# Kernel tuning notes

Hardware: AMD Instinct MI355X
Metric: run time of the kernel (lower is better)

## Reference

```python
import jax, jax.numpy as jnp
import numpy as np

N_NODES = 50000
N_EDGES = 800000
N_GRAPHS = 512
NEG_SLOPE = 0.2  # PyG GATConv default LeakyReLU slope


def _gat_layer(x, src, dst, W, a_src, a_dst, b, n_nodes):
    """PyG-style GATConv (concat=True, self-loops already in src/dst)."""
    H, C = a_src.shape
    h = (x @ W).reshape(n_nodes, H, C)            # [N, H, C]
    e_s = (h * a_src).sum(-1)                     # [N, H]
    e_d = (h * a_dst).sum(-1)                     # [N, H]
    e = jax.nn.leaky_relu(e_s[src] + e_d[dst], NEG_SLOPE)  # [E, H]
    # segment softmax over destination nodes
    m = jax.ops.segment_max(e, dst, num_segments=n_nodes)
    w = jnp.exp(e - m[dst])
    s = jax.ops.segment_sum(w, dst, num_segments=n_nodes)
    alpha = w / (s[dst] + 1e-16)                  # [E, H]
    out = jax.ops.segment_sum(h[src] * alpha[:, :, None], dst, num_segments=n_nodes)
    return out.reshape(n_nodes, H * C) + b


def setup_inputs() -> dict:
    key = jax.random.key(0)
    ks = jax.random.split(key, 16)
    x = jax.random.normal(ks[0], (N_NODES, 2), dtype=jnp.float32)
    edge_index = jax.random.randint(ks[1], (2, N_EDGES), 0, N_NODES, dtype=jnp.int64 if jax.config.jax_enable_x64 else jnp.int32)
    batch = jnp.sort(jax.random.randint(ks[2], (N_NODES,), 0, N_GRAPHS))
    g = lambda k, shape: (jax.random.normal(k, shape, dtype=jnp.float32) * 0.1)
    return {
        "x": x, "edge_index": edge_index, "batch": batch,
        "W1": g(ks[3], (2, 64)),   "a1s": g(ks[4], (8, 8)),  "a1d": g(ks[5], (8, 8)),  "b1": jnp.zeros((64,), jnp.float32),
        "W2": g(ks[6], (64, 128)), "a2s": g(ks[7], (8, 16)), "a2d": g(ks[8], (8, 16)), "b2": jnp.zeros((128,), jnp.float32),
        "W3": g(ks[9], (128, 128)),"a3s": g(ks[10], (8, 16)),"a3d": g(ks[11], (8, 16)),"b3": jnp.zeros((128,), jnp.float32),
        "fc1W": g(ks[12], (128, 32)), "fc1b": jnp.zeros((32,), jnp.float32),
        "fc2W": g(ks[13], (32, 10)),  "fc2b": jnp.zeros((10,), jnp.float32),
    }


def reference(x, edge_index, batch, W1, a1s, a1d, b1, W2, a2s, a2d, b2, W3, a3s, a3d, b3, fc1W, fc1b, fc2W, fc2b):
    n = x.shape[0]
    loop = jnp.arange(n, dtype=edge_index.dtype)
    src = jnp.concatenate([edge_index[0], loop])  # add self-loops (PyG default)
    dst = jnp.concatenate([edge_index[1], loop])
    h = jax.nn.elu(_gat_layer(x, src, dst, W1, a1s, a1d, b1, n))
    h = jax.nn.elu(_gat_layer(h, src, dst, W2, a2s, a2d, b2, n))
    h = _gat_layer(h, src, dst, W3, a3s, a3d, b3, n)
    # global mean pool over graphs
    sums = jax.ops.segment_sum(h, batch, num_segments=N_GRAPHS)
    cnt = jax.ops.segment_sum(jnp.ones((n,), h.dtype), batch, num_segments=N_GRAPHS)
    pooled = sums / jnp.maximum(cnt, 1.0)[:, None]   # [G, 128]
    z = jax.nn.relu(pooled @ fc1W + fc1b)
    return jax.nn.log_softmax(z @ fc2W + fc2b, axis=1)
```

## Files before the change

### kernel.cpp

```cpp
#include <hip/hip_runtime.h>
#include <cstddef>
#include <cstdint>

typedef __attribute__((ext_vector_type(8))) short bf16x8;
typedef __attribute__((ext_vector_type(4))) float floatx4;
typedef __attribute__((ext_vector_type(2))) float v2f;


__device__ __forceinline__ unsigned bf16pair(float a, float b) {
    unsigned ua = __float_as_uint(a), ub = __float_as_uint(b);
    ua += 0x7fffu + ((ua >> 16) & 1u);
    ub += 0x7fffu + ((ub >> 16) & 1u);
    return (ua >> 16) | (ub & 0xffff0000u);
}
__device__ __forceinline__ unsigned short bf16one(float a) {
    unsigned ua = __float_as_uint(a);
    ua += 0x7fffu + ((ua >> 16) & 1u);
    return (unsigned short)(ua >> 16);
}

#define BSTRIDE 8192


__global__ __launch_bounds__(256) void prep_k(
    const int* __restrict__ edge, unsigned* __restrict__ barr,
    int* __restrict__ bcnt, int E, int EA, int B1,
    const float* __restrict__ W2, unsigned short* __restrict__ Wt2,
    const float* __restrict__ W3, unsigned short* __restrict__ Wt3,
    const float* __restrict__ x, const float* __restrict__ W1,
    const float* __restrict__ a1s, const float* __restrict__ a1d,
    unsigned char* __restrict__ h8a, float* __restrict__ es,
    float* __restrict__ ed, int N) {
    int tid = threadIdx.x;
    if ((int)blockIdx.x < B1) {
        __shared__ int h[256];
        __shared__ int lbase[256];
        h[tid] = 0;
        __syncthreads();
        int start = blockIdx.x * 4096;
        unsigned ent[16];
        int lp[16];
#pragma unroll
        for (int k = 0; k < 16; ++k) {
            int i = start + k * 256 + tid;
            if (i < EA) {
                int s, d;
                if (i < E) { s = edge[i]; d = edge[E + i]; }
                else { s = i - E; d = s; }
                int b = d >> 8;
                ent[k] = (unsigned)s | ((unsigned)(d & 255) << 16) | ((unsigned)b << 24);
                lp[k] = atomicAdd(&h[b], 1);
            } else {
                ent[k] = 0xffffffffu;
                lp[k] = 0;
            }
        }
        __syncthreads();
        lbase[tid] = h[tid] ? atomicAdd(&bcnt[tid], h[tid]) : 0;
        __syncthreads();
#pragma unroll
        for (int k = 0; k < 16; ++k) {
            if (ent[k] != 0xffffffffu) {
                int b = ent[k] >> 24;
                int pos = lbase[b] + lp[k];
                if (pos < BSTRIDE)
                    barr[(size_t)b * BSTRIDE + pos] = ent[k] & 0x00ffffffu;
            }
        }
        return;
    }
    if ((int)blockIdx.x < B1 + 96) {
        int rel = blockIdx.x - B1;
        const float* W = (rel < 32) ? W2 : W3;
        unsigned short* Wt = (rel < 32) ? Wt2 : Wt3;
        int total = (rel < 32) ? 8192 : 16384;
        int o = ((rel < 32) ? rel : rel - 32) * 256 + tid;
        if (o < total) {
            int j = o & 7, lane = (o >> 3) & 63, ct = (o >> 9) & 7, ks = o >> 12;
            int k = ks * 32 + (lane >> 4) * 8 + j;
            int n = ct * 16 + (lane & 15);
            Wt[o] = bf16one(W[k * 128 + n]);
        }
        return;
    }
    int wave = tid >> 6, lane = tid & 63;
    int nbase = (blockIdx.x - B1 - 96) * 32;
    float w0 = W1[lane], w1 = W1[64 + lane];
    float as = a1s[lane], ad = a1d[lane];
    int head = lane >> 3;
#pragma unroll
    for (int it = 0; it < 8; ++it) {
        int n = nbase + it * 4 + wave;
        int nc = (n < N) ? n : N - 1;
        float2 xv = ((const float2*)x)[nc];
        float h = xv.x * w0 + xv.y * w1;
        float ps = h * as, pd = h * ad;
#pragma unroll
        for (int off = 1; off < 8; off <<= 1) {
            ps += __shfl_xor(ps, off);
            pd += __shfl_xor(pd, off);
        }
        if (n < N) {
            unsigned d = __builtin_amdgcn_cvt_pk_fp8_f32(h, h, 0, false);
            h8a[(size_t)n * 64 + lane] = (unsigned char)d;
            if ((lane & 7) == 0) { es[n * 8 + head] = ps; ed[n * 8 + head] = pd; }
        }
    }
}


__global__ __launch_bounds__(256) void bucket2_k(const unsigned* __restrict__ barr,
                                                 const int* __restrict__ bcnt,
                                                 int* __restrict__ offsets,
                                                 int* __restrict__ esrc,
                                                 int N, int EA, int nbuck) {
    __shared__ int sd[256];
    __shared__ int bb[256];
    __shared__ int cur[256];
    int b = blockIdx.x, tid = threadIdx.x;
    int v = (tid < nbuck) ? bcnt[tid] : 0;
    sd[tid] = v;
    __syncthreads();
    for (int off = 1; off < 256; off <<= 1) {
        int t = (tid >= off) ? sd[tid - off] : 0;
        __syncthreads();
        sd[tid] += t;
        __syncthreads();
    }
    bb[tid] = sd[tid] - v;
    __syncthreads();
    int bbase = bb[b];
    if (b == 0 && tid == 0) offsets[N] = EA;
    if (b == 0 && tid < 8) esrc[EA + tid] = 0;

    int cnt = bcnt[b];
    const unsigned* arr = barr + (size_t)b * BSTRIDE;
    sd[tid] = 0;
    __syncthreads();
    for (int i = tid; i < cnt; i += 256)
        atomicAdd(&sd[(arr[i] >> 16) & 0xff], 1);
    __syncthreads();
    v = sd[tid];
    for (int off = 1; off < 256; off <<= 1) {
        int t = (tid >= off) ? sd[tid - off] : 0;
        __syncthreads();
        sd[tid] += t;
        __syncthreads();
    }
    int base = bbase + sd[tid] - v;
    int n = b * 256 + tid;
    if (n < N) offsets[n] = base;
    cur[tid] = base;
    __syncthreads();
    for (int i = tid; i < cnt; i += 256) {
        unsigned e = arr[i];
        int pos = atomicAdd(&cur[(e >> 16) & 0xff], 1);
        esrc[pos] = (int)(e & 0xffffu);
    }
}


template <int IN>
__global__ __launch_bounds__(256) void gemm_mfma_k(
    const unsigned short* __restrict__ a16, const unsigned short* __restrict__ Wt,
    const float* __restrict__ a_s, const float* __restrict__ a_d,
    unsigned char* __restrict__ h8, float* __restrict__ es, float* __restrict__ ed,
    int n_nodes) {
    constexpr int KSTEPS = IN / 32;
    __shared__ float Cl[64 * 132];
    int wave = threadIdx.x >> 6, lane = threadIdx.x & 63;
    int q = lane >> 4, m = lane & 15;
    int rbase = blockIdx.x * 64;

    floatx4 acc[8];
#pragma unroll
    for (int ct = 0; ct < 8; ++ct) acc[ct] = (floatx4){0.f, 0.f, 0.f, 0.f};

    int ra = rbase + wave * 16 + m;
    if (ra >= n_nodes) ra = n_nodes - 1;
    const unsigned short* arow = a16 + (size_t)ra * IN + q * 8;

#pragma unroll
    for (int ks = 0; ks < KSTEPS; ++ks) {
        bf16x8 af = *(const bf16x8*)(arow + ks * 32);
        const unsigned short* wp = Wt + ((size_t)(ks * 8) * 64 + lane) * 8;
#pragma unroll
        for (int ct = 0; ct < 8; ++ct) {
            bf16x8 bf = *(const bf16x8*)(wp + (size_t)ct * 64 * 8);
            acc[ct] = __builtin_amdgcn_mfma_f32_16x16x32_bf16(af, bf, acc[ct], 0, 0, 0);
        }
    }

#pragma unroll
    for (int ct = 0; ct < 8; ++ct)
#pragma unroll
        for (int i = 0; i < 4; ++i)
            Cl[(wave * 16 + q * 4 + i) * 132 + ct * 16 + m] = acc[ct][i];
    __syncthreads();

    int rl = threadIdx.x >> 2, part = threadIdx.x & 3;
    int r = rbase + rl;
    if (r < n_nodes) {
        const float* cp = &Cl[rl * 132 + part * 32];
        float e0s = 0.f, e0d = 0.f, e1s = 0.f, e1d = 0.f;
#pragma unroll
        for (int c = 0; c < 16; ++c) {
            float v = cp[c];
            int ai = part * 32 + c;
            e0s += v * a_s[ai];
            e0d += v * a_d[ai];
        }
#pragma unroll
        for (int c = 16; c < 32; ++c) {
            float v = cp[c];
            int ai = part * 32 + c;
            e1s += v * a_s[ai];
            e1d += v * a_d[ai];
        }
        unsigned pk8[8];
#pragma unroll
        for (int u = 0; u < 8; ++u) {
            unsigned d = __builtin_amdgcn_cvt_pk_fp8_f32(cp[4 * u], cp[4 * u + 1], 0, false);
            d = __builtin_amdgcn_cvt_pk_fp8_f32(cp[4 * u + 2], cp[4 * u + 3], d, true);
            pk8[u] = d;
        }
        uint4* hp = (uint4*)(h8 + (size_t)r * 128) + part * 2;
        hp[0] = make_uint4(pk8[0], pk8[1], pk8[2], pk8[3]);
        hp[1] = make_uint4(pk8[4], pk8[5], pk8[6], pk8[7]);
        es[r * 8 + 2 * part] = e0s;
        es[r * 8 + 2 * part + 1] = e1s;
        ed[r * 8 + 2 * part] = e0d;
        ed[r * 8 + 2 * part + 1] = e1d;
    }
}


template <int NCOL, bool ELU>
__global__ __launch_bounds__(256) void gat_k(
    const unsigned char* __restrict__ hsrc, const float* __restrict__ es,
    const float* __restrict__ ed, const int* __restrict__ offsets,
    const int* __restrict__ esrc, const float* __restrict__ bias,
    void* __restrict__ outp, int n_nodes) {
    constexpr int UPL = NCOL / 16;
    int wave = threadIdx.x >> 6, lane = threadIdx.x & 63;
    int half = lane >> 5;
    int hl = lane & 31;
    int slot = hl >> 3;
    int l = lane & 7;
    int n = blockIdx.x * 8 + wave * 2 + half;
    bool valid = (n < n_nodes);
    int nc = valid ? n : 0;
    float edn = ed[nc * 8 + l];
    int start = valid ? offsets[nc] : 0;
    int end = valid ? offsets[nc + 1] : 0;

    v2f acc2[UPL];
#pragma unroll
    for (int k = 0; k < UPL; ++k) acc2[k] = (v2f){0.f, 0.f};
    float s = 0.f;

    for (int j = start; j < end; j += 4) {
        int jj = j + slot;
        bool act = (jj < end);
        int src = esrc[jj];
        float e0 = es[(size_t)src * 8 + l] + edn;
        float e = fmaxf(e0, 0.2f * e0);
        float p = act ? __expf(e) : 0.f;
        s += p;
        v2f p2 = (v2f){p, p};
        if constexpr (NCOL == 128) {
            uint4 u = *(const uint4*)(hsrc + (size_t)src * 128 + 16 * l);
            acc2[0] += p2 * (v2f)__builtin_amdgcn_cvt_pk_f32_fp8(u.x, false);
            acc2[1] += p2 * (v2f)__builtin_amdgcn_cvt_pk_f32_fp8(u.x, true);
            acc2[2] += p2 * (v2f)__builtin_amdgcn_cvt_pk_f32_fp8(u.y, false);
            acc2[3] += p2 * (v2f)__builtin_amdgcn_cvt_pk_f32_fp8(u.y, true);
            acc2[4] += p2 * (v2f)__builtin_amdgcn_cvt_pk_f32_fp8(u.z, false);
            acc2[5] += p2 * (v2f)__builtin_amdgcn_cvt_pk_f32_fp8(u.z, true);
            acc2[6] += p2 * (v2f)__builtin_amdgcn_cvt_pk_f32_fp8(u.w, false);
            acc2[7] += p2 * (v2f)__builtin_amdgcn_cvt_pk_f32_fp8(u.w, true);
        } else {
            uint2 u = *(const uint2*)(hsrc + (size_t)src * 64 + 8 * l);
            acc2[0] += p2 * (v2f)__builtin_amdgcn_cvt_pk_f32_fp8(u.x, false);
            acc2[1] += p2 * (v2f)__builtin_amdgcn_cvt_pk_f32_fp8(u.x, true);
            acc2[2] += p2 * (v2f)__builtin_amdgcn_cvt_pk_f32_fp8(u.y, false);
            acc2[3] += p2 * (v2f)__builtin_amdgcn_cvt_pk_f32_fp8(u.y, true);
        }
    }

    s += __shfl_xor(s, 8);
    s += __shfl_xor(s, 16);
    float v[2 * UPL];
#pragma unroll
    for (int k = 0; k < UPL; ++k) { v[2 * k] = acc2[k].x; v[2 * k + 1] = acc2[k].y; }
#pragma unroll
    for (int k = 0; k < 2 * UPL; ++k) {
        v[k] += __shfl_xor(v[k], 8);
        v[k] += __shfl_xor(v[k], 16);
    }

    if (slot == 0 && valid) {
        float r = 1.f / (s + 1e-16f);
#pragma unroll
        for (int k = 0; k < 2 * UPL; ++k) {
            float b = bias[(2 * UPL) * l + k];
            float t = v[k] * r + b;
            if constexpr (ELU) t = (t > 0.f) ? t : expm1f(t);
            v[k] = t;
        }
        if constexpr (NCOL == 128) {
            uint4* op = (uint4*)outp + (size_t)n * 16 + 2 * l;
            op[0] = make_uint4(bf16pair(v[0], v[1]), bf16pair(v[2], v[3]),
                               bf16pair(v[4], v[5]), bf16pair(v[6], v[7]));
            op[1] = make_uint4(bf16pair(v[8], v[9]), bf16pair(v[10], v[11]),
                               bf16pair(v[12], v[13]), bf16pair(v[14], v[15]));
        } else {
            ((uint4*)outp)[(size_t)n * 8 + l] =
                make_uint4(bf16pair(v[0], v[1]), bf16pair(v[2], v[3]),
                           bf16pair(v[4], v[5]), bf16pair(v[6], v[7]));
        }
    }
}


__global__ __launch_bounds__(64) void pool_k(const unsigned* __restrict__ hu,
                                             const int* __restrict__ batch,
                                             float* __restrict__ sums,
                                             float* __restrict__ cnt, int n_nodes) {
    int c = threadIdx.x;
    int base = blockIdx.x * 32;
    float a0 = 0.f, a1 = 0.f, cacc = 0.f;
    int gprev = -1;
    for (int k = 0; k < 32; k++) {
        int n = base + k;
        if (n >= n_nodes) break;
        int g = batch[n];
        if (g != gprev) {
            if (gprev >= 0) {
                atomicAdd(&sums[gprev * 128 + 2 * c], a0);
                atomicAdd(&sums[gprev * 128 + 2 * c + 1], a1);
                if (c == 0) atomicAdd(&cnt[gprev], cacc);
            }
            a0 = 0.f; a1 = 0.f; cacc = 0.f; gprev = g;
        }
        unsigned u = hu[(size_t)n * 64 + c];
        a0 += __uint_as_float(u << 16);
        a1 += __uint_as_float(u & 0xffff0000u);
        cacc += 1.f;
    }
    if (gprev >= 0) {
        atomicAdd(&sums[gprev * 128 + 2 * c], a0);
        atomicAdd(&sums[gprev * 128 + 2 * c + 1], a1);
        if (c == 0) atomicAdd(&cnt[gprev], cacc);
    }
}


__global__ __launch_bounds__(64) void fc_k(const float* __restrict__ sums,
                                           const float* __restrict__ cnt,
                                           const float* __restrict__ fc1W,
                                           const float* __restrict__ fc1b,
                                           const float* __restrict__ fc2W,
                                           const float* __restrict__ fc2b,
                                           float* __restrict__ out) {
    int g = blockIdx.x, lane = threadIdx.x;
    __shared__ float p[128];
    __shared__ float z[32];
    __shared__ float logits[10];
    float inv = 1.f / fmaxf(cnt[g], 1.f);
    p[lane] = sums[g * 128 + lane] * inv;
    p[lane + 64] = sums[g * 128 + 64 + lane] * inv;
    __syncthreads();
    if (lane < 32) {
        float a = fc1b[lane];
        for (int k = 0; k < 128; k++) a += p[k] * fc1W[k * 32 + lane];
        z[lane] = fmaxf(a, 0.f);
    }
    __syncthreads();
    if (lane < 10) {
        float a = fc2b[lane];
        for (int k = 0; k < 32; k++) a += z[k] * fc2W[k * 10 + lane];
        logits[lane] = a;
    }
    __syncthreads();
    if (lane < 10) {
        float mx = logits[0];
#pragma unroll
        for (int i = 1; i < 10; i++) mx = fmaxf(mx, logits[i]);
        float se = 0.f;
#pragma unroll
        for (int i = 0; i < 10; i++) se += __expf(logits[i] - mx);
        out[g * 10 + lane] = logits[lane] - mx - logf(se);
    }
}


extern "C" void kernel_launch(void* const* d_in, const int* in_sizes, int n_in,
                              void* d_out, int out_size, void* d_ws, size_t ws_size,
                              hipStream_t stream) {
    const float* x = (const float*)d_in[0];
    const int* edge = (const int*)d_in[1];
    const int* batch = (const int*)d_in[2];
    const float* W1 = (const float*)d_in[3];
    const float* a1s = (const float*)d_in[4];
    const float* a1d = (const float*)d_in[5];
    const float* b1 = (const float*)d_in[6];
    const float* W2 = (const float*)d_in[7];
    const float* a2s = (const float*)d_in[8];
    const float* a2d = (const float*)d_in[9];
    const float* b2 = (const float*)d_in[10];
    const float* W3 = (const float*)d_in[11];
    const float* a3s = (const float*)d_in[12];
    const float* a3d = (const float*)d_in[13];
    const float* b3 = (const float*)d_in[14];
    const float* fc1W = (const float*)d_in[15];
    const float* fc1b = (const float*)d_in[16];
    const float* fc2W = (const float*)d_in[17];
    const float* fc2b = (const float*)d_in[18];
    float* out = (float*)d_out;

    const int N = in_sizes[0] / 2;
    const int E = in_sizes[1] / 2;
    const int EA = E + N;
    const int NG = out_size / 10;
    const int NBUCK = (N + 255) >> 8;
    const int B1 = (EA + 4095) / 4096;
    const int G1 = (N + 31) / 32;

    char* p = (char*)d_ws;
    unsigned* h3b16 = (unsigned*)p; p += (size_t)N * 64 * 4;
    unsigned char* h8 = (unsigned char*)p; p += (size_t)N * 128;
    unsigned char* h8a = (unsigned char*)p; p += (size_t)N * 64;
    unsigned short* a16a = (unsigned short*)p; p += (size_t)N * 64 * 2;
    unsigned short* a16b = (unsigned short*)p; p += (size_t)N * 128 * 2;
    unsigned short* Wt2 = (unsigned short*)p; p += (size_t)64 * 128 * 2;
    unsigned short* Wt3 = (unsigned short*)p; p += (size_t)128 * 128 * 2;
    float* es = (float*)p;  p += (size_t)N * 8 * 4;
    float* ed = (float*)p;  p += (size_t)N * 8 * 4;
    float* sums = (float*)p; p += (size_t)NG * 128 * 4;
    float* cnt = (float*)p;  p += (size_t)NG * 4;
    int* bcnt = (int*)p;     p += 256 * 4;
    int* offsets = (int*)p;  p += (size_t)(N + 1) * 4;
    int* esrc = (int*)p;     p += (size_t)(EA + 8) * 4;
    unsigned* barr = (unsigned*)p; p += (size_t)NBUCK * BSTRIDE * 4;

    hipMemsetAsync(sums, 0, ((size_t)NG * 128 + NG + 256) * 4, stream);

    prep_k<<<B1 + 96 + G1, 256, 0, stream>>>(
        edge, barr, bcnt, E, EA, B1, W2, Wt2, W3, Wt3,
        x, W1, a1s, a1d, h8a, es, ed, N);
    bucket2_k<<<NBUCK, 256, 0, stream>>>(barr, bcnt, offsets, esrc, N, EA, NBUCK);

    int mblocks = (N + 63) / 64;
    int ablocks = (N + 7) / 8;
    gat_k<64, true><<<ablocks, 256, 0, stream>>>(h8a, es, ed, offsets, esrc, b1, a16a, N);
    gemm_mfma_k<64><<<mblocks, 256, 0, stream>>>(a16a, Wt2, a2s, a2d, h8, es, ed, N);
    gat_k<128, true><<<ablocks, 256, 0, stream>>>(h8, es, ed, offsets, esrc, b2, a16b, N);
    gemm_mfma_k<128><<<mblocks, 256, 0, stream>>>(a16b, Wt3, a3s, a3d, h8, es, ed, N);
    gat_k<128, false><<<ablocks, 256, 0, stream>>>(h8, es, ed, offsets, esrc, b3, h3b16, N);

    pool_k<<<(N + 31) / 32, 64, 0, stream>>>(h3b16, batch, sums, cnt, N);
    fc_k<<<NG, 64, 0, stream>>>(sums, cnt, fc1W, fc1b, fc2W, fc2b, out);
}
```

Baseline: 278.3 us.

## Fuse all stages into one cooperative persistent kernel with grid syncs

```diff
diff --git a/kernel.cpp b/kernel.cpp
--- a/kernel.cpp
+++ b/kernel.cpp
@@ -1,10 +1,16 @@
 #include <hip/hip_runtime.h>
+#include <hip/hip_cooperative_groups.h>
 #include <cstddef>
 #include <cstdint>
+
+namespace cg = cooperative_groups;
 
 typedef __attribute__((ext_vector_type(8))) short bf16x8;
 typedef __attribute__((ext_vector_type(4))) float floatx4;
 typedef __attribute__((ext_vector_type(2))) float v2f;
+
+#define BSTRIDE 8192
+#define SMEM_BYTES (64 * 132 * 4)
 
 
 __device__ __forceinline__ unsigned bf16pair(float a, float b) {
@@ -19,34 +25,46 @@
     return (unsigned short)(ua >> 16);
 }
 
-#define BSTRIDE 8192
-
-
-__global__ __launch_bounds__(256) void prep_k(
-    const int* __restrict__ edge, unsigned* __restrict__ barr,
-    int* __restrict__ bcnt, int E, int EA, int B1,
-    const float* __restrict__ W2, unsigned short* __restrict__ Wt2,
-    const float* __restrict__ W3, unsigned short* __restrict__ Wt3,
-    const float* __restrict__ x, const float* __restrict__ W1,
-    const float* __restrict__ a1s, const float* __restrict__ a1d,
-    unsigned char* __restrict__ h8a, float* __restrict__ es,
-    float* __restrict__ ed, int N) {
+
+struct MA {
+    const int* edge;
+    unsigned* barr;
+    int* bcnt;
+    int E, EA, B1, PREP, NBUCK, N, NG, ablocks, mblocks, pblocks;
+    const float *W1, *W2, *W3;
+    unsigned short *Wt2, *Wt3;
+    const float* x;
+    const float *a1s, *a1d, *a2s, *a2d, *a3s, *a3d;
+    const float *b1, *b2, *b3;
+    unsigned char *h8a, *h8;
+    unsigned short *a16a, *a16b;
+    unsigned* h3b16;
+    float *es, *ed;
+    int *offsets, *esrc;
+    const int* batch;
+    float *sums, *cnt;
+    const float *fc1W, *fc1b, *fc2W, *fc2b;
+    float* out;
+};
+
+
+__device__ void prep_body(int vb, const MA& a, char* smem) {
     int tid = threadIdx.x;
-    if ((int)blockIdx.x < B1) {
-        __shared__ int h[256];
-        __shared__ int lbase[256];
+    if (vb < a.B1) {
+        int* h = (int*)smem;
+        int* lbase = h + 256;
         h[tid] = 0;
         __syncthreads();
-        int start = blockIdx.x * 4096;
+        int start = vb * 4096;
         unsigned ent[16];
         int lp[16];
 #pragma unroll
         for (int k = 0; k < 16; ++k) {
             int i = start + k * 256 + tid;
-            if (i < EA) {
+            if (i < a.EA) {
                 int s, d;
-                if (i < E) { s = edge[i]; d = edge[E + i]; }
-                else { s = i - E; d = s; }
+                if (i < a.E) { s = a.edge[i]; d = a.edge[a.E + i]; }
+                else { s = i - a.E; d = s; }
                 int b = d >> 8;
                 ent[k] = (unsigned)s | ((unsigned)(d & 255) << 16) | ((unsigned)b << 24);
                 lp[k] = atomicAdd(&h[b], 1);
@@ -56,7 +74,7 @@
             }
         }
         __syncthreads();
-        lbase[tid] = h[tid] ? atomicAdd(&bcnt[tid], h[tid]) : 0;
+        lbase[tid] = h[tid] ? atomicAdd(&a.bcnt[tid], h[tid]) : 0;
         __syncthreads();
 #pragma unroll
         for (int k = 0; k < 16; ++k) {
@@ -64,15 +82,16 @@
                 int b = ent[k] >> 24;
                 int pos = lbase[b] + lp[k];
                 if (pos < BSTRIDE)
-                    barr[(size_t)b * BSTRIDE + pos] = ent[k] & 0x00ffffffu;
+                    a.barr[(size_t)b * BSTRIDE + pos] = ent[k] & 0x00ffffffu;
             }
         }
+        __syncthreads();
         return;
     }
-    if ((int)blockIdx.x < B1 + 96) {
-        int rel = blockIdx.x - B1;
-        const float* W = (rel < 32) ? W2 : W3;
-        unsigned short* Wt = (rel < 32) ? Wt2 : Wt3;
+    if (vb < a.B1 + 96) {
+        int rel = vb - a.B1;
+        const float* W = (rel < 32) ? a.W2 : a.W3;
+        unsigned short* Wt = (rel < 32) ? a.Wt2 : a.Wt3;
         int total = (rel < 32) ? 8192 : 16384;
         int o = ((rel < 32) ? rel : rel - 32) * 256 + tid;
         if (o < total) {
@@ -84,15 +103,15 @@
         return;
     }
     int wave = tid >> 6, lane = tid & 63;
-    int nbase = (blockIdx.x - B1 - 96) * 32;
-    float w0 = W1[lane], w1 = W1[64 + lane];
-    float as = a1s[lane], ad = a1d[lane];
+    int nbase = (vb - a.B1 - 96) * 32;
+    float w0 = a.W1[lane], w1 = a.W1[64 + lane];
+    float as = a.a1s[lane], ad = a.a1d[lane];
     int head = lane >> 3;
 #pragma unroll
     for (int it = 0; it < 8; ++it) {
         int n = nbase + it * 4 + wave;
-        int nc = (n < N) ? n : N - 1;
-        float2 xv = ((const float2*)x)[nc];
+        int nc = (n < a.N) ? n : a.N - 1;
+        float2 xv = ((const float2*)a.x)[nc];
         float h = xv.x * w0 + xv.y * w1;
         float ps = h * as, pd = h * ad;
 #pragma unroll
@@ -100,25 +119,20 @@
             ps += __shfl_xor(ps, off);
             pd += __shfl_xor(pd, off);
         }
-        if (n < N) {
+        if (n < a.N) {
             unsigned d = __builtin_amdgcn_cvt_pk_fp8_f32(h, h, 0, false);
-            h8a[(size_t)n * 64 + lane] = (unsigned char)d;
-            if ((lane & 7) == 0) { es[n * 8 + head] = ps; ed[n * 8 + head] = pd; }
-        }
-    }
-}
-
-
-__global__ __launch_bounds__(256) void bucket2_k(const unsigned* __restrict__ barr,
-                                                 const int* __restrict__ bcnt,
-                                                 int* __restrict__ offsets,
-                                                 int* __restrict__ esrc,
-                                                 int N, int EA, int nbuck) {
-    __shared__ int sd[256];
-    __shared__ int bb[256];
-    __shared__ int cur[256];
-    int b = blockIdx.x, tid = threadIdx.x;
-    int v = (tid < nbuck) ? bcnt[tid] : 0;
+            a.h8a[(size_t)n * 64 + lane] = (unsigned char)d;
+            if ((lane & 7) == 0) { a.es[n * 8 + head] = ps; a.ed[n * 8 + head] = pd; }
+        }
+    }
+}
+
+__device__ void bucket2_body(int b, const MA& a, char* smem) {
+    int* sd = (int*)smem;
+    int* bb = sd + 256;
+    int* cur = bb + 256;
+    int tid = threadIdx.x;
+    int v = (tid < a.NBUCK) ? a.bcnt[tid] : 0;
     sd[tid] = v;
     __syncthreads();
     for (int off = 1; off < 256; off <<= 1) {
@@ -130,11 +144,11 @@
     bb[tid] = sd[tid] - v;
     __syncthreads();
     int bbase = bb[b];
-    if (b == 0 && tid == 0) offsets[N] = EA;
-    if (b == 0 && tid < 8) esrc[EA + tid] = 0;
-
-    int cnt = bcnt[b];
-    const unsigned* arr = barr + (size_t)b * BSTRIDE;
+    if (b == 0 && tid == 0) a.offsets[a.N] = a.EA;
+    if (b == 0 && tid < 8) a.esrc[a.EA + tid] = 0;
+
+    int cnt = a.bcnt[b];
+    const unsigned* arr = a.barr + (size_t)b * BSTRIDE;
     sd[tid] = 0;
     __syncthreads();
     for (int i = tid; i < cnt; i += 256)
@@ -149,105 +163,30 @@
     }
     int base = bbase + sd[tid] - v;
     int n = b * 256 + tid;
-    if (n < N) offsets[n] = base;
+    if (n < a.N) a.offsets[n] = base;
     cur[tid] = base;
     __syncthreads();
     for (int i = tid; i < cnt; i += 256) {
         unsigned e = arr[i];
         int pos = atomicAdd(&cur[(e >> 16) & 0xff], 1);
-        esrc[pos] = (int)(e & 0xffffu);
-    }
-}
-
-
-template <int IN>
-__global__ __launch_bounds__(256) void gemm_mfma_k(
-    const unsigned short* __restrict__ a16, const unsigned short* __restrict__ Wt,
-    const float* __restrict__ a_s, const float* __restrict__ a_d,
-    unsigned char* __restrict__ h8, float* __restrict__ es, float* __restrict__ ed,
-    int n_nodes) {
-    constexpr int KSTEPS = IN / 32;
-    __shared__ float Cl[64 * 132];
-    int wave = threadIdx.x >> 6, lane = threadIdx.x & 63;
-    int q = lane >> 4, m = lane & 15;
-    int rbase = blockIdx.x * 64;
-
-    floatx4 acc[8];
-#pragma unroll
-    for (int ct = 0; ct < 8; ++ct) acc[ct] = (floatx4){0.f, 0.f, 0.f, 0.f};
-
-    int ra = rbase + wave * 16 + m;
-    if (ra >= n_nodes) ra = n_nodes - 1;
-    const unsigned short* arow = a16 + (size_t)ra * IN + q * 8;
-
-#pragma unroll
-    for (int ks = 0; ks < KSTEPS; ++ks) {
-        bf16x8 af = *(const bf16x8*)(arow + ks * 32);
-        const unsigned short* wp = Wt + ((size_t)(ks * 8) * 64 + lane) * 8;
-#pragma unroll
-        for (int ct = 0; ct < 8; ++ct) {
-            bf16x8 bf = *(const bf16x8*)(wp + (size_t)ct * 64 * 8);
-            acc[ct] = __builtin_amdgcn_mfma_f32_16x16x32_bf16(af, bf, acc[ct], 0, 0, 0);
-        }
-    }
-
-#pragma unroll
-    for (int ct = 0; ct < 8; ++ct)
-#pragma unroll
-        for (int i = 0; i < 4; ++i)
-            Cl[(wave * 16 + q * 4 + i) * 132 + ct * 16 + m] = acc[ct][i];
-    __syncthreads();
-
-    int rl = threadIdx.x >> 2, part = threadIdx.x & 3;
-    int r = rbase + rl;
-    if (r < n_nodes) {
-        const float* cp = &Cl[rl * 132 + part * 32];
-        float e0s = 0.f, e0d = 0.f, e1s = 0.f, e1d = 0.f;
-#pragma unroll
-        for (int c = 0; c < 16; ++c) {
-            float v = cp[c];
-            int ai = part * 32 + c;
-            e0s += v * a_s[ai];
-            e0d += v * a_d[ai];
-        }
-#pragma unroll
-        for (int c = 16; c < 32; ++c) {
-            float v = cp[c];
-            int ai = part * 32 + c;
-            e1s += v * a_s[ai];
-            e1d += v * a_d[ai];
-        }
-        unsigned pk8[8];
-#pragma unroll
-        for (int u = 0; u < 8; ++u) {
-            unsigned d = __builtin_amdgcn_cvt_pk_fp8_f32(cp[4 * u], cp[4 * u + 1], 0, false);
-            d = __builtin_amdgcn_cvt_pk_fp8_f32(cp[4 * u + 2], cp[4 * u + 3], d, true);
-            pk8[u] = d;
-        }
-        uint4* hp = (uint4*)(h8 + (size_t)r * 128) + part * 2;
-        hp[0] = make_uint4(pk8[0], pk8[1], pk8[2], pk8[3]);
-        hp[1] = make_uint4(pk8[4], pk8[5], pk8[6], pk8[7]);
-        es[r * 8 + 2 * part] = e0s;
-        es[r * 8 + 2 * part + 1] = e1s;
-        ed[r * 8 + 2 * part] = e0d;
-        ed[r * 8 + 2 * part + 1] = e1d;
-    }
-}
-
+        a.esrc[pos] = (int)(e & 0xffffu);
+    }
+    __syncthreads();
+}
 
 template <int NCOL, bool ELU>
-__global__ __launch_bounds__(256) void gat_k(
-    const unsigned char* __restrict__ hsrc, const float* __restrict__ es,
-    const float* __restrict__ ed, const int* __restrict__ offsets,
-    const int* __restrict__ esrc, const float* __restrict__ bias,
-    void* __restrict__ outp, int n_nodes) {
+__device__ void gat_body(int vb, const unsigned char* __restrict__ hsrc,
+                         const float* __restrict__ es, const float* __restrict__ ed,
+                         const int* __restrict__ offsets, const int* __restrict__ esrc,
+                         const float* __restrict__ bias, void* __restrict__ outp,
+                         int n_nodes) {
     constexpr int UPL = NCOL / 16;
     int wave = threadIdx.x >> 6, lane = threadIdx.x & 63;
     int half = lane >> 5;
     int hl = lane & 31;
     int slot = hl >> 3;
     int l = lane & 7;
-    int n = blockIdx.x * 8 + wave * 2 + half;
+    int n = vb * 8 + wave * 2 + half;
     bool valid = (n < n_nodes);
     int nc = valid ? n : 0;
     float edn = ed[nc * 8 + l];
@@ -321,143 +260,280 @@
     }
 }
 
-
-__global__ __launch_bounds__(64) void pool_k(const unsigned* __restrict__ hu,
-                                             const int* __restrict__ batch,
-                                             float* __restrict__ sums,
-                                             float* __restrict__ cnt, int n_nodes) {
+template <int IN>
+__device__ void mfma_body(int vb, const unsigned short* __restrict__ a16,
+                          const unsigned short* __restrict__ Wt,
+                          const float* __restrict__ a_s, const float* __restrict__ a_d,
+                          unsigned char* __restrict__ h8, float* __restrict__ es,
+                          float* __restrict__ ed, int n_nodes, char* smem) {
+    constexpr int KSTEPS = IN / 32;
+    float* Cl = (float*)smem;
+    int wave = threadIdx.x >> 6, lane = threadIdx.x & 63;
+    int q = lane >> 4, m = lane & 15;
+    int rbase = vb * 64;
+
+    floatx4 acc[8];
+#pragma unroll
+    for (int ct = 0; ct < 8; ++ct) acc[ct] = (floatx4){0.f, 0.f, 0.f, 0.f};
+
+    int ra = rbase + wave * 16 + m;
+    if (ra >= n_nodes) ra = n_nodes - 1;
+    const unsigned short* arow = a16 + (size_t)ra * IN + q * 8;
+
+#pragma unroll
+    for (int ks = 0; ks < KSTEPS; ++ks) {
+        bf16x8 af = *(const bf16x8*)(arow + ks * 32);
+        const unsigned short* wp = Wt + ((size_t)(ks * 8) * 64 + lane) * 8;
+#pragma unroll
+        for (int ct = 0; ct < 8; ++ct) {
+            bf16x8 bf = *(const bf16x8*)(wp + (size_t)ct * 64 * 8);
+            acc[ct] = __builtin_amdgcn_mfma_f32_16x16x32_bf16(af, bf, acc[ct], 0, 0, 0);
+        }
+    }
+
+#pragma unroll
+    for (int ct = 0; ct < 8; ++ct)
+#pragma unroll
+        for (int i = 0; i < 4; ++i)
+            Cl[(wave * 16 + q * 4 + i) * 132 + ct * 16 + m] = acc[ct][i];
+    __syncthreads();
+
+    int rl = threadIdx.x >> 2, part = threadIdx.x & 3;
+    int r = rbase + rl;
+    if (r < n_nodes) {
+        const float* cp = &Cl[rl * 132 + part * 32];
+        float e0s = 0.f, e0d = 0.f, e1s = 0.f, e1d = 0.f;
+#pragma unroll
+        for (int c = 0; c < 16; ++c) {
+            float v = cp[c];
+            int ai = part * 32 + c;
+            e0s += v * a_s[ai];
+            e0d += v * a_d[ai];
+        }
+#pragma unroll
+        for (int c = 16; c < 32; ++c) {
+            float v = cp[c];
+            int ai = part * 32 + c;
+            e1s += v * a_s[ai];
+            e1d += v * a_d[ai];
+        }
+        unsigned pk8[8];
+#pragma unroll
+        for (int u = 0; u < 8; ++u) {
+            unsigned d = __builtin_amdgcn_cvt_pk_fp8_f32(cp[4 * u], cp[4 * u + 1], 0, false);
+            d = __builtin_amdgcn_cvt_pk_fp8_f32(cp[4 * u + 2], cp[4 * u + 3], d, true);
+            pk8[u] = d;
+        }
+        uint4* hp = (uint4*)(h8 + (size_t)r * 128) + part * 2;
+        hp[0] = make_uint4(pk8[0], pk8[1], pk8[2], pk8[3]);
+        hp[1] = make_uint4(pk8[4], pk8[5], pk8[6], pk8[7]);
+        es[r * 8 + 2 * part] = e0s;
+        es[r * 8 + 2 * part + 1] = e1s;
+        ed[r * 8 + 2 * part] = e0d;
+        ed[r * 8 + 2 * part + 1] = e1d;
+    }
+    __syncthreads();
+}
+
+__device__ void pool_body(int vb, const MA& a) {
     int c = threadIdx.x;
-    int base = blockIdx.x * 32;
+    if (c >= 64) return;
+    int base = vb * 32;
     float a0 = 0.f, a1 = 0.f, cacc = 0.f;
     int gprev = -1;
     for (int k = 0; k < 32; k++) {
         int n = base + k;
-        if (n >= n_nodes) break;
-        int g = batch[n];
+        if (n >= a.N) break;
+        int g = a.batch[n];
         if (g != gprev) {
             if (gprev >= 0) {
-                atomicAdd(&sums[gprev * 128 + 2 * c], a0);
-                atomicAdd(&sums[gprev * 128 + 2 * c + 1], a1);
-                if (c == 0) atomicAdd(&cnt[gprev], cacc);
+                atomicAdd(&a.sums[gprev * 128 + 2 * c], a0);
+                atomicAdd(&a.sums[gprev * 128 + 2 * c + 1], a1);
+                if (c == 0) atomicAdd(&a.cnt[gprev], cacc);
             }
             a0 = 0.f; a1 = 0.f; cacc = 0.f; gprev = g;
         }
-        unsigned u = hu[(size_t)n * 64 + c];
+        unsigned u = a.h3b16[(size_t)n * 64 + c];
         a0 += __uint_as_float(u << 16);
         a1 += __uint_as_float(u & 0xffff0000u);
         cacc += 1.f;
     }
     if (gprev >= 0) {
-        atomicAdd(&sums[gprev * 128 + 2 * c], a0);
-        atomicAdd(&sums[gprev * 128 + 2 * c + 1], a1);
-        if (c == 0) atomicAdd(&cnt[gprev], cacc);
-    }
-}
-
-
-__global__ __launch_bounds__(64) void fc_k(const float* __restrict__ sums,
-                                           const float* __restrict__ cnt,
-                                           const float* __restrict__ fc1W,
-                                           const float* __restrict__ fc1b,
-                                           const float* __restrict__ fc2W,
-                                           const float* __restrict__ fc2b,
-                                           float* __restrict__ out) {
-    int g = blockIdx.x, lane = threadIdx.x;
-    __shared__ float p[128];
-    __shared__ float z[32];
-    __shared__ float logits[10];
-    float inv = 1.f / fmaxf(cnt[g], 1.f);
-    p[lane] = sums[g * 128 + lane] * inv;
-    p[lane + 64] = sums[g * 128 + 64 + lane] * inv;
-    __syncthreads();
-    if (lane < 32) {
-        float a = fc1b[lane];
-        for (int k = 0; k < 128; k++) a += p[k] * fc1W[k * 32 + lane];
-        z[lane] = fmaxf(a, 0.f);
-    }
-    __syncthreads();
-    if (lane < 10) {
-        float a = fc2b[lane];
-        for (int k = 0; k < 32; k++) a += z[k] * fc2W[k * 10 + lane];
-        logits[lane] = a;
-    }
-    __syncthreads();
-    if (lane < 10) {
+        atomicAdd(&a.sums[gprev * 128 + 2 * c], a0);
+        atomicAdd(&a.sums[gprev * 128 + 2 * c + 1], a1);
+        if (c == 0) atomicAdd(&a.cnt[gprev], cacc);
+    }
+}
+
+__device__ void fc_body(int g, const MA& a, char* smem) {
+    float* p = (float*)smem;
+    float* z = p + 128;
+    float* logits = z + 32;
+    int tid = threadIdx.x;
+    if (tid < 64) {
+        float inv = 1.f / fmaxf(a.cnt[g], 1.f);
+        p[tid] = a.sums[g * 128 + tid] * inv;
+        p[tid + 64] = a.sums[g * 128 + 64 + tid] * inv;
+    }
+    __syncthreads();
+    if (tid < 32) {
+        float acc = a.fc1b[tid];
+        for (int k = 0; k < 128; k++) acc += p[k] * a.fc1W[k * 32 + tid];
+        z[tid] = fmaxf(acc, 0.f);
+    }
+    __syncthreads();
+    if (tid < 10) {
+        float acc = a.fc2b[tid];
+        for (int k = 0; k < 32; k++) acc += z[k] * a.fc2W[k * 10 + tid];
+        logits[tid] = acc;
+    }
+    __syncthreads();
+    if (tid < 10) {
         float mx = logits[0];
 #pragma unroll
         for (int i = 1; i < 10; i++) mx = fmaxf(mx, logits[i]);
         float se = 0.f;
 #pragma unroll
         for (int i = 0; i < 10; i++) se += __expf(logits[i] - mx);
-        out[g * 10 + lane] = logits[lane] - mx - logf(se);
-    }
+        a.out[g * 10 + tid] = logits[tid] - mx - logf(se);
+    }
+    __syncthreads();
+}
+
+
+__global__ __launch_bounds__(256) void mega_k(MA a) {
+    __shared__ __align__(16) char smem[SMEM_BYTES];
+    cg::grid_group grid = cg::this_grid();
+
+    for (int vb = blockIdx.x; vb < a.PREP; vb += gridDim.x) prep_body(vb, a, smem);
+    grid.sync();
+    for (int vb = blockIdx.x; vb < a.NBUCK; vb += gridDim.x) bucket2_body(vb, a, smem);
+    grid.sync();
+    for (int vb = blockIdx.x; vb < a.ablocks; vb += gridDim.x)
+        gat_body<64, true>(vb, a.h8a, a.es, a.ed, a.offsets, a.esrc, a.b1, a.a16a, a.N);
+    grid.sync();
+    for (int vb = blockIdx.x; vb < a.mblocks; vb += gridDim.x)
+        mfma_body<64>(vb, a.a16a, a.Wt2, a.a2s, a.a2d, a.h8, a.es, a.ed, a.N, smem);
+    grid.sync();
+    for (int vb = blockIdx.x; vb < a.ablocks; vb += gridDim.x)
+        gat_body<128, true>(vb, a.h8, a.es, a.ed, a.offsets, a.esrc, a.b2, a.a16b, a.N);
+    grid.sync();
+    for (int vb = blockIdx.x; vb < a.mblocks; vb += gridDim.x)
+        mfma_body<128>(vb, a.a16b, a.Wt3, a.a3s, a.a3d, a.h8, a.es, a.ed, a.N, smem);
+    grid.sync();
+    for (int vb = blockIdx.x; vb < a.ablocks; vb += gridDim.x)
+        gat_body<128, false>(vb, a.h8, a.es, a.ed, a.offsets, a.esrc, a.b3, a.h3b16, a.N);
+    grid.sync();
+    for (int vb = blockIdx.x; vb < a.pblocks; vb += gridDim.x) pool_body(vb, a);
+    grid.sync();
+    for (int vb = blockIdx.x; vb < a.NG; vb += gridDim.x) fc_body(vb, a, smem);
+}
+
+
+__global__ __launch_bounds__(256) void prep_w(MA a) {
+    __shared__ __align__(16) char smem[2048];
+    prep_body(blockIdx.x, a, smem);
+}
+__global__ __launch_bounds__(256) void bucket2_w(MA a) {
+    __shared__ __align__(16) char smem[3072];
+    bucket2_body(blockIdx.x, a, smem);
+}
+template <int NCOL, bool ELU>
+__global__ __launch_bounds__(256) void gat_w(MA a, const unsigned char* h,
+                                             const float* bias, void* outp) {
+    gat_body<NCOL, ELU>(blockIdx.x, h, a.es, a.ed, a.offsets, a.esrc, bias, outp, a.N);
+}
+template <int IN>
+__global__ __launch_bounds__(256) void mfma_w(MA a, const unsigned short* a16,
+                                              const unsigned short* Wt,
+                                              const float* a_s, const float* a_d) {
+    __shared__ __align__(16) char smem[SMEM_BYTES];
+    mfma_body<IN>(blockIdx.x, a16, Wt, a_s, a_d, a.h8, a.es, a.ed, a.N, smem);
+}
+__global__ __launch_bounds__(64) void pool_w(MA a) { pool_body(blockIdx.x, a); }
+__global__ __launch_bounds__(256) void fc_w(MA a) {
+    __shared__ __align__(16) char smem[1024];
+    fc_body(blockIdx.x, a, smem);
 }
 
 
 extern "C" void kernel_launch(void* const* d_in, const int* in_sizes, int n_in,
                               void* d_out, int out_size, void* d_ws, size_t ws_size,
                               hipStream_t stream) {
-    const float* x = (const float*)d_in[0];
-    const int* edge = (const int*)d_in[1];
-    const int* batch = (const int*)d_in[2];
-    const float* W1 = (const float*)d_in[3];
-    const float* a1s = (const float*)d_in[4];
-    const float* a1d = (const float*)d_in[5];
-    const float* b1 = (const float*)d_in[6];
-    const float* W2 = (const float*)d_in[7];
-    const float* a2s = (const float*)d_in[8];
-    const float* a2d = (const float*)d_in[9];
-    const float* b2 = (const float*)d_in[10];
-    const float* W3 = (const float*)d_in[11];
-    const float* a3s = (const float*)d_in[12];
-    const float* a3d = (const float*)d_in[13];
-    const float* b3 = (const float*)d_in[14];
-    const float* fc1W = (const float*)d_in[15];
-    const float* fc1b = (const float*)d_in[16];
-    const float* fc2W = (const float*)d_in[17];
-    const float* fc2b = (const float*)d_in[18];
-    float* out = (float*)d_out;
+    MA a;
+    a.x = (const float*)d_in[0];
+    a.edge = (const int*)d_in[1];
+    a.batch = (const int*)d_in[2];
+    a.W1 = (const float*)d_in[3];
+    a.a1s = (const float*)d_in[4];
+    a.a1d = (const float*)d_in[5];
+    a.b1 = (const float*)d_in[6];
+    a.W2 = (const float*)d_in[7];
+    a.a2s = (const float*)d_in[8];
+    a.a2d = (const float*)d_in[9];
+    a.b2 = (const float*)d_in[10];
+    a.W3 = (const float*)d_in[11];
+    a.a3s = (const float*)d_in[12];
+    a.a3d = (const float*)d_in[13];
+    a.b3 = (const float*)d_in[14];
+    a.fc1W = (const float*)d_in[15];
+    a.fc1b = (const float*)d_in[16];
+    a.fc2W = (const float*)d_in[17];
+    a.fc2b = (const float*)d_in[18];
+    a.out = (float*)d_out;
 
     const int N = in_sizes[0] / 2;
     const int E = in_sizes[1] / 2;
     const int EA = E + N;
-    const int NG = out_size / 10;
-    const int NBUCK = (N + 255) >> 8;
-    const int B1 = (EA + 4095) / 4096;
-    const int G1 = (N + 31) / 32;
+    a.N = N; a.E = E; a.EA = EA;
+    a.NG = out_size / 10;
+    a.NBUCK = (N + 255) >> 8;
+    a.B1 = (EA + 4095) / 4096;
+    a.PREP = a.B1 + 96 + (N + 31) / 32;
+    a.ablocks = (N + 7) / 8;
+    a.mblocks = (N + 63) / 64;
+    a.pblocks = (N + 31) / 32;
 
     char* p = (char*)d_ws;
-    unsigned* h3b16 = (unsigned*)p; p += (size_t)N * 64 * 4;
-    unsigned char* h8 = (unsigned char*)p; p += (size_t)N * 128;
-    unsigned char* h8a = (unsigned char*)p; p += (size_t)N * 64;
-    unsigned short* a16a = (unsigned short*)p; p += (size_t)N * 64 * 2;
-    unsigned short* a16b = (unsigned short*)p; p += (size_t)N * 128 * 2;
-    unsigned short* Wt2 = (unsigned short*)p; p += (size_t)64 * 128 * 2;
-    unsigned short* Wt3 = (unsigned short*)p; p += (size_t)128 * 128 * 2;
-    float* es = (float*)p;  p += (size_t)N * 8 * 4;
-    float* ed = (float*)p;  p += (size_t)N * 8 * 4;
-    float* sums = (float*)p; p += (size_t)NG * 128 * 4;
-    float* cnt = (float*)p;  p += (size_t)NG * 4;
-    int* bcnt = (int*)p;     p += 256 * 4;
-    int* offsets = (int*)p;  p += (size_t)(N + 1) * 4;
-    int* esrc = (int*)p;     p += (size_t)(EA + 8) * 4;
-    unsigned* barr = (unsigned*)p; p += (size_t)NBUCK * BSTRIDE * 4;
-
-    hipMemsetAsync(sums, 0, ((size_t)NG * 128 + NG + 256) * 4, stream);
-
-    prep_k<<<B1 + 96 + G1, 256, 0, stream>>>(
-        edge, barr, bcnt, E, EA, B1, W2, Wt2, W3, Wt3,
-        x, W1, a1s, a1d, h8a, es, ed, N);
-    bucket2_k<<<NBUCK, 256, 0, stream>>>(barr, bcnt, offsets, esrc, N, EA, NBUCK);
-
-    int mblocks = (N + 63) / 64;
-    int ablocks = (N + 7) / 8;
-    gat_k<64, true><<<ablocks, 256, 0, stream>>>(h8a, es, ed, offsets, esrc, b1, a16a, N);
-    gemm_mfma_k<64><<<mblocks, 256, 0, stream>>>(a16a, Wt2, a2s, a2d, h8, es, ed, N);
-    gat_k<128, true><<<ablocks, 256, 0, stream>>>(h8, es, ed, offsets, esrc, b2, a16b, N);
-    gemm_mfma_k<128><<<mblocks, 256, 0, stream>>>(a16b, Wt3, a3s, a3d, h8, es, ed, N);
-    gat_k<128, false><<<ablocks, 256, 0, stream>>>(h8, es, ed, offsets, esrc, b3, h3b16, N);
-
-    pool_k<<<(N + 31) / 32, 64, 0, stream>>>(h3b16, batch, sums, cnt, N);
-    fc_k<<<NG, 64, 0, stream>>>(sums, cnt, fc1W, fc1b, fc2W, fc2b, out);
-}
+    a.h3b16 = (unsigned*)p; p += (size_t)N * 64 * 4;
+    a.h8 = (unsigned char*)p; p += (size_t)N * 128;
+    a.h8a = (unsigned char*)p; p += (size_t)N * 64;
+    a.a16a = (unsigned short*)p; p += (size_t)N * 64 * 2;
+    a.a16b = (unsigned short*)p; p += (size_t)N * 128 * 2;
+    a.Wt2 = (unsigned short*)p; p += (size_t)64 * 128 * 2;
+    a.Wt3 = (unsigned short*)p; p += (size_t)128 * 128 * 2;
+    a.es = (float*)p;  p += (size_t)N * 8 * 4;
+    a.ed = (float*)p;  p += (size_t)N * 8 * 4;
+    a.sums = (float*)p; p += (size_t)a.NG * 128 * 4;
+    a.cnt = (float*)p;  p += (size_t)a.NG * 4;
+    a.bcnt = (int*)p;   p += 256 * 4;
+    a.offsets = (int*)p; p += (size_t)(N + 1) * 4;
+    a.esrc = (int*)p;    p += (size_t)(EA + 8) * 4;
+    a.barr = (unsigned*)p; p += (size_t)a.NBUCK * BSTRIDE * 4;
+
+    hipMemsetAsync(a.sums, 0, ((size_t)a.NG * 128 + a.NG + 256) * 4, stream);
+
+    int maxb = 0;
+    hipError_t qe = hipOccupancyMaxActiveBlocksPerMultiprocessor(
+        &maxb, (const void*)mega_k, 256, 0);
+    bool coop_ok = (qe == hipSuccess && maxb > 0);
+    if (coop_ok) {
+        int grid = maxb * 256;
+        if (grid > 2048) grid = 2048;
+        void* args[] = { &a };
+        hipError_t le = hipLaunchCooperativeKernel(
+            (const void*)mega_k, dim3(grid), dim3(256), args, 0, stream);
+        coop_ok = (le == hipSuccess);
+    }
+    if (!coop_ok) {
+        prep_w<<<a.PREP, 256, 0, stream>>>(a);
+        bucket2_w<<<a.NBUCK, 256, 0, stream>>>(a);
+        gat_w<64, true><<<a.ablocks, 256, 0, stream>>>(a, a.h8a, a.b1, a.a16a);
+        mfma_w<64><<<a.mblocks, 256, 0, stream>>>(a, a.a16a, a.Wt2, a.a2s, a.a2d);
+        gat_w<128, true><<<a.ablocks, 256, 0, stream>>>(a, a.h8, a.b2, a.a16b);
+        mfma_w<128><<<a.mblocks, 256, 0, stream>>>(a, a.a16b, a.Wt3, a.a3s, a.a3d);
+        gat_w<128, false><<<a.ablocks, 256, 0, stream>>>(a, a.h8, a.b3, a.h3b16);
+        pool_w<<<a.pblocks, 64, 0, stream>>>(a);
+        fc_w<<<a.NG, 256, 0, stream>>>(a);
+    }
+}
```

New measurement: 942.5 us. 239% more time.
